# Performance work log

Hardware: AMD Instinct MI355X
Metric: run time of the kernel (lower is better)

The kernel has to match this reference:

```python
import jax, jax.numpy as jnp
import numpy as np

P_SCALE = 5.0
Q_SCALE = 0.3
EPS = 1e-06
NORM_EPS = 1e-12


def stack3x3_same(img):
    """im2col for 3x3 kernel, 'same' zero padding, stride 1.
    img: (B,H,W,C) -> (B,H,W,9,C), tap order row-major (dy,dx) in {-1,0,1}^2,
    matching the TF stack3x3 ordering with clip=0, pad=1."""
    B, H, W, C = img.shape
    padded = jnp.pad(img, ((0, 0), (1, 1), (1, 1), (0, 0)))
    taps = [padded[:, dy:dy + H, dx:dx + W, :] for dy in range(3) for dx in range(3)]
    return jnp.stack(taps, axis=3)


def setup_inputs() -> dict:
    key = jax.random.key(0)
    k1, k2 = jax.random.split(key)
    B, H, W, C = 32, 64, 64, 64
    n_kernels, ksize = 128, 3
    inputs = jax.random.normal(k1, (B, H, W, C), dtype=jnp.float32)
    # glorot-uniform-ish weight, shape (1, C*k*k, n_kernels)
    fan_in = C * ksize * ksize
    limit = np.sqrt(6.0 / (fan_in + n_kernels)).astype(np.float32)
    w = jax.random.uniform(k2, (1, fan_in, n_kernels), dtype=jnp.float32,
                           minval=-limit, maxval=limit)
    p = jnp.full((n_kernels,), 0.7 * P_SCALE, dtype=jnp.float32)
    q = jnp.full((1,), 1.0 * Q_SCALE, dtype=jnp.float32)
    return {"inputs": inputs, "w": w, "p": p, "q": q}


def reference(inputs, w, p, q):
    B, H, W, C = inputs.shape
    n_kernels = w.shape[-1]
    ksq = w.shape[1] // C  # kernel_size^2 = 9

    # im2col: (B, H*W, C*9), tap-major flatten (matches tf stack axis=3 + reshape)
    x = stack3x3_same(inputs).reshape(B, H * W, ksq * C)

    p_eff = jnp.exp(p / P_SCALE)            # (n_kernels,)
    q_eff = jnp.exp(-q / Q_SCALE)           # (1,)

    # L2 norms (sqrt of clamped square-sum), matching l2_normal
    x_norm = jnp.sqrt(jnp.maximum(jnp.sum(x * x, axis=2, keepdims=True), NORM_EPS)) + q_eff
    w_norm = jnp.sqrt(jnp.maximum(jnp.sum(w * w, axis=1, keepdims=True), NORM_EPS))

    # cosine-similarity matmul: (B, HW, K) x (1, K, N) -> (B, HW, N)
    sim = jnp.einsum('bsk,kn->bsn', x / x_norm, (w / w_norm)[0])

    # sharpened rescaling: sign(x) * (|x| + eps)^p
    out = jnp.sign(sim) * jnp.power(jnp.abs(sim) + EPS, p_eff)
    return out.reshape(B, H, W, n_kernels)
```

## Files before the change

kernel.cpp:

```cpp
#include <hip/hip_runtime.h>
#include <hip/hip_bf16.h>


typedef short bf16x8 __attribute__((ext_vector_type(8)));
typedef float f32x4 __attribute__((ext_vector_type(4)));

__device__ __forceinline__ unsigned short f2bf(float f) {
    union { float f; unsigned int u; } v; v.f = f;
    unsigned int u = v.u;
    unsigned int r = (u + 0x7fffu + ((u >> 16) & 1u)) >> 16;
    return (unsigned short)r;
}

__global__ void prep_w_kernel(const float* __restrict__ w,
                              unsigned short* __restrict__ wn2) {
    const int n = blockIdx.x;
    const int lane = threadIdx.x;
    float vals[9];
    float s = 0.f;
#pragma unroll
    for (int i = 0; i < 9; ++i) {
        float v = w[(i * 64 + lane) * 128 + n];
        vals[i] = v;
        s += v * v;
    }
#pragma unroll
    for (int off = 1; off < 64; off <<= 1) s += __shfl_xor(s, off);
    const float inv = 1.0f / sqrtf(fmaxf(s, 1e-12f));
    const int kc = lane >> 5, koff = lane & 31;
#pragma unroll
    for (int i = 0; i < 9; ++i)
        wn2[((i * 2 + kc) * 128 + n) * 32 + koff] = f2bf(vals[i] * inv);
}

__global__ __launch_bounds__(256, 4) void cossim_main(
    const float* __restrict__ in, const unsigned short* __restrict__ wn,
    const float* __restrict__ p, const float* __restrict__ q,
    float* __restrict__ out) {
    __shared__ unsigned short A[4 * 66 * 72];
    __shared__ float rcsum[256];
    __shared__ float xni[128];
    __shared__ float pfs[128];

    const int tid = (int)threadIdx.x;
    const int l = ((int)blockIdx.x & 7) * 128 + ((int)blockIdx.x >> 3);
    const int b = l >> 5, y0 = (l & 31) * 2;

    if (tid < 128) pfs[tid] = expf(p[tid] * 0.2f);

    {
        const int r = tid >> 6;
        const int col = tid & 63;
        const int row = y0 + r - 1;
        unsigned short* dst = &A[(r * 66 + col + 1) * 72];
        float s = 0.f;
        if ((unsigned)row < 64u) {
            const float4* src = reinterpret_cast<const float4*>(
                in + (size_t)b * 262144 + row * 4096 + col * 64);
#pragma unroll
            for (int it = 0; it < 8; ++it) {
                float4 v0 = src[2 * it];
                float4 v1 = src[2 * it + 1];
                s += v0.x * v0.x + v0.y * v0.y + v0.z * v0.z + v0.w * v0.w;
                s += v1.x * v1.x + v1.y * v1.y + v1.z * v1.z + v1.w * v1.w;
                union { float f; unsigned u; } ux, uy, uz, uw;
                uint4 pk;
                ux.f = v0.x; uy.f = v0.y; uz.f = v0.z; uw.f = v0.w;
                pk.x = __builtin_amdgcn_perm(uy.u + 0x8000u, ux.u + 0x8000u, 0x07060302u);
                pk.y = __builtin_amdgcn_perm(uw.u + 0x8000u, uz.u + 0x8000u, 0x07060302u);
                ux.f = v1.x; uy.f = v1.y; uz.f = v1.z; uw.f = v1.w;
                pk.z = __builtin_amdgcn_perm(uy.u + 0x8000u, ux.u + 0x8000u, 0x07060302u);
                pk.w = __builtin_amdgcn_perm(uw.u + 0x8000u, uz.u + 0x8000u, 0x07060302u);
                *reinterpret_cast<uint4*>(dst + it * 8) = pk;
            }
        } else {
            uint4 z; z.x = z.y = z.z = z.w = 0u;
#pragma unroll
            for (int it = 0; it < 8; ++it)
                *reinterpret_cast<uint4*>(dst + it * 8) = z;
        }
        rcsum[tid] = s;
    }
    if (tid < 64) {
        const int r = tid >> 4, side = (tid >> 3) & 1, ch = (tid & 7) * 8;
        uint4 z; z.x = z.y = z.z = z.w = 0u;
        *reinterpret_cast<uint4*>(&A[(r * 66 + side * 65) * 72 + ch]) = z;
    }
    __syncthreads();

    if (tid < 128) {
        const int ry = tid >> 6, x = tid & 63;
        const float qe = expf(q[0] * (-1.0f / 0.3f));
        float s = 0.f;
#pragma unroll
        for (int dy = 0; dy < 3; ++dy) {
            const float* rs = &rcsum[(ry + dy) * 64];
            if (x > 0) s += rs[x - 1];
            s += rs[x];
            if (x < 63) s += rs[x + 1];
        }
        xni[tid] = 1.0f / (sqrtf(fmaxf(s, 1e-12f)) + qe);
    }
    __syncthreads();

    const int wv = tid >> 6, lane = tid & 63;
    const int lr = lane & 15, lg = lane >> 4;
    const int wm = wv >> 1, wnh = wv & 1;
    f32x4 acc[4][4] = {};
    const unsigned short* wB = wn + (wnh * 64 + lr) * 32 + lg * 8;

    bf16x8 bc0 = *reinterpret_cast<const bf16x8*>(wB);
    bf16x8 bc1 = *reinterpret_cast<const bf16x8*>(wB + 512);
    bf16x8 bc2 = *reinterpret_cast<const bf16x8*>(wB + 1024);
    bf16x8 bc3 = *reinterpret_cast<const bf16x8*>(wB + 1536);

#pragma unroll
    for (int s = 0; s < 18; ++s) {
        bf16x8 bn0, bn1, bn2, bn3;
        if (s + 1 < 18) {
            const unsigned short* wt = wB + (s + 1) * 4096;
            bn0 = *reinterpret_cast<const bf16x8*>(wt);
            bn1 = *reinterpret_cast<const bf16x8*>(wt + 512);
            bn2 = *reinterpret_cast<const bf16x8*>(wt + 1024);
            bn3 = *reinterpret_cast<const bf16x8*>(wt + 1536);
        }
        const int dy = s / 6, dx = (s >> 1) % 3, kc = s & 1;
        const unsigned short* abase =
            &A[((wm + dy) * 66 + lr + dx) * 72 + kc * 32 + lg * 8];
#pragma unroll
        for (int mf = 0; mf < 4; ++mf) {
            bf16x8 av = *reinterpret_cast<const bf16x8*>(abase + mf * 16 * 72);
            acc[mf][0] = __builtin_amdgcn_mfma_f32_16x16x32_bf16(av, bc0, acc[mf][0], 0, 0, 0);
            acc[mf][1] = __builtin_amdgcn_mfma_f32_16x16x32_bf16(av, bc1, acc[mf][1], 0, 0, 0);
            acc[mf][2] = __builtin_amdgcn_mfma_f32_16x16x32_bf16(av, bc2, acc[mf][2], 0, 0, 0);
            acc[mf][3] = __builtin_amdgcn_mfma_f32_16x16x32_bf16(av, bc3, acc[mf][3], 0, 0, 0);
        }
        bc0 = bn0; bc1 = bn1; bc2 = bn2; bc3 = bn3;
    }

    float* orow = out + ((size_t)(b * 64 + y0 + wm) * 64) * 128;
#pragma unroll
    for (int mf = 0; mf < 4; ++mf) {
#pragma unroll
        for (int i = 0; i < 4; ++i) {
            const int pix = mf * 16 + lg * 4 + i;
            const float xn = xni[wm * 64 + pix];
#pragma unroll
            for (int nf = 0; nf < 4; ++nf) {
                const int n = wnh * 64 + nf * 16 + lr;
                float sim = acc[mf][nf][i] * xn;
                float aa = fabsf(sim) + 1e-6f;
                float r = exp2f(pfs[n] * log2f(aa));
                orow[(size_t)pix * 128 + n] = copysignf(r, sim);
            }
        }
    }
}

extern "C" void kernel_launch(void* const* d_in, const int* in_sizes, int n_in,
                              void* d_out, int out_size, void* d_ws, size_t ws_size,
                              hipStream_t stream) {
    (void)in_sizes; (void)n_in; (void)out_size; (void)ws_size;
    const float* in = (const float*)d_in[0];
    const float* w  = (const float*)d_in[1];
    const float* p  = (const float*)d_in[2];
    const float* q  = (const float*)d_in[3];
    float* out = (float*)d_out;
    unsigned short* wn = (unsigned short*)d_ws;

    prep_w_kernel<<<128, 64, 0, stream>>>(w, wn);
    cossim_main<<<1024, 256, 0, stream>>>(in, wn, p, q, out);
}
```

Measured before the change: 43.35 us.

## Use two waves per block with each wave computing both rows

Halves the block to 128 threads. Each wave now covers both output rows (8 M-fragments) for one 64-column half of the output channels, instead of one row per wave. Each weight fragment is reused across twice as many A fragments, which cuts global weight loads per MFMA. The cost is a doubled accumulator (128 floats per lane), so register pressure rises and occupancy falls, and the staging loop runs twice per thread.

```diff
diff --git a/kernel.cpp b/kernel.cpp
--- a/kernel.cpp
+++ b/kernel.cpp
@@ -33,7 +33,7 @@
         wn2[((i * 2 + kc) * 128 + n) * 32 + koff] = f2bf(vals[i] * inv);
 }
 
-__global__ __launch_bounds__(256, 4) void cossim_main(
+__global__ __launch_bounds__(128, 2) void cossim_main(
     const float* __restrict__ in, const unsigned short* __restrict__ wn,
     const float* __restrict__ p, const float* __restrict__ q,
     float* __restrict__ out) {
@@ -46,11 +46,13 @@
     const int l = ((int)blockIdx.x & 7) * 128 + ((int)blockIdx.x >> 3);
     const int b = l >> 5, y0 = (l & 31) * 2;
 
-    if (tid < 128) pfs[tid] = expf(p[tid] * 0.2f);
+    pfs[tid] = expf(p[tid] * 0.2f);
 
-    {
-        const int r = tid >> 6;
-        const int col = tid & 63;
+#pragma unroll
+    for (int u2 = 0; u2 < 2; ++u2) {
+        const int u = tid + u2 * 128;
+        const int r = u >> 6;
+        const int col = u & 63;
         const int row = y0 + r - 1;
         unsigned short* dst = &A[(r * 66 + col + 1) * 72];
         float s = 0.f;
@@ -79,7 +81,7 @@
             for (int it = 0; it < 8; ++it)
                 *reinterpret_cast<uint4*>(dst + it * 8) = z;
         }
-        rcsum[tid] = s;
+        rcsum[u] = s;
     }
     if (tid < 64) {
         const int r = tid >> 4, side = (tid >> 3) & 1, ch = (tid & 7) * 8;
@@ -88,7 +90,7 @@
     }
     __syncthreads();
 
-    if (tid < 128) {
+    {
         const int ry = tid >> 6, x = tid & 63;
         const float qe = expf(q[0] * (-1.0f / 0.3f));
         float s = 0.f;
@@ -105,9 +107,8 @@
 
     const int wv = tid >> 6, lane = tid & 63;
     const int lr = lane & 15, lg = lane >> 4;
-    const int wm = wv >> 1, wnh = wv & 1;
-    f32x4 acc[4][4] = {};
-    const unsigned short* wB = wn + (wnh * 64 + lr) * 32 + lg * 8;
+    f32x4 acc[8][4] = {};
+    const unsigned short* wB = wn + (wv * 64 + lr) * 32 + lg * 8;
 
     bf16x8 bc0 = *reinterpret_cast<const bf16x8*>(wB);
     bf16x8 bc1 = *reinterpret_cast<const bf16x8*>(wB + 512);
@@ -125,11 +126,12 @@
             bn3 = *reinterpret_cast<const bf16x8*>(wt + 1536);
         }
         const int dy = s / 6, dx = (s >> 1) % 3, kc = s & 1;
-        const unsigned short* abase =
-            &A[((wm + dy) * 66 + lr + dx) * 72 + kc * 32 + lg * 8];
 #pragma unroll
-        for (int mf = 0; mf < 4; ++mf) {
-            bf16x8 av = *reinterpret_cast<const bf16x8*>(abase + mf * 16 * 72);
+        for (int mf = 0; mf < 8; ++mf) {
+            const unsigned short* ap =
+                &A[(((mf >> 2) + dy) * 66 + (mf & 3) * 16 + lr + dx) * 72
+                   + kc * 32 + lg * 8];
+            bf16x8 av = *reinterpret_cast<const bf16x8*>(ap);
             acc[mf][0] = __builtin_amdgcn_mfma_f32_16x16x32_bf16(av, bc0, acc[mf][0], 0, 0, 0);
             acc[mf][1] = __builtin_amdgcn_mfma_f32_16x16x32_bf16(av, bc1, acc[mf][1], 0, 0, 0);
             acc[mf][2] = __builtin_amdgcn_mfma_f32_16x16x32_bf16(av, bc2, acc[mf][2], 0, 0, 0);
@@ -138,20 +140,22 @@
         bc0 = bn0; bc1 = bn1; bc2 = bn2; bc3 = bn3;
     }
 
-    float* orow = out + ((size_t)(b * 64 + y0 + wm) * 64) * 128;
+    const float* pf = &pfs[wv * 64];
 #pragma unroll
-    for (int mf = 0; mf < 4; ++mf) {
+    for (int mf = 0; mf < 8; ++mf) {
+        float* orow = out + ((size_t)(b * 64 + y0 + (mf >> 2)) * 64) * 128 + wv * 64;
 #pragma unroll
         for (int i = 0; i < 4; ++i) {
             const int pix = mf * 16 + lg * 4 + i;
-            const float xn = xni[wm * 64 + pix];
+            const int px = pix & 63;
+            const float xn = xni[pix];
 #pragma unroll
             for (int nf = 0; nf < 4; ++nf) {
-                const int n = wnh * 64 + nf * 16 + lr;
+                const int n = nf * 16 + lr;
                 float sim = acc[mf][nf][i] * xn;
                 float aa = fabsf(sim) + 1e-6f;
-                float r = exp2f(pfs[n] * log2f(aa));
-                orow[(size_t)pix * 128 + n] = copysignf(r, sim);
+                float r = exp2f(pf[n] * log2f(aa));
+                orow[(size_t)px * 128 + n] = copysignf(r, sim);
             }
         }
     }
@@ -169,5 +173,5 @@
     unsigned short* wn = (unsigned short*)d_ws;
 
     prep_w_kernel<<<128, 64, 0, stream>>>(w, wn);
-    cossim_main<<<1024, 256, 0, stream>>>(in, wn, p, q, out);
+    cossim_main<<<1024, 128, 0, stream>>>(in, wn, p, q, out);
 }
```

Result: slower. 51.21 us (+18.1%).

## Split output channels across blocks and stage output through LDS for coalesced stores

Applied to the files above, without the earlier changes.

Each block now handles only half of the 128 output channels, doubling the grid to 2048 blocks and halving the accumulator registers per wave. Results are staged in shared memory (reusing the A tile buffer) and then written with float4 stores covering contiguous 64-channel rows, in place of scattered scalar stores. The cost is that every input tile is loaded, converted to bf16 and norm-reduced twice, once per channel-half block, and two extra barriers are added.

```diff
diff --git a/kernel.cpp b/kernel.cpp
--- a/kernel.cpp
+++ b/kernel.cpp
@@ -33,20 +33,25 @@
         wn2[((i * 2 + kc) * 128 + n) * 32 + koff] = f2bf(vals[i] * inv);
 }
 
+#define OBLD 68
+
 __global__ __launch_bounds__(256, 4) void cossim_main(
     const float* __restrict__ in, const unsigned short* __restrict__ wn,
     const float* __restrict__ p, const float* __restrict__ q,
     float* __restrict__ out) {
-    __shared__ unsigned short A[4 * 66 * 72];
+    __shared__ __align__(16) unsigned char smemRaw[4 * 66 * 72 * 2];
+    unsigned short* A = reinterpret_cast<unsigned short*>(smemRaw);
+    float* OB = reinterpret_cast<float*>(smemRaw);
     __shared__ float rcsum[256];
     __shared__ float xni[128];
-    __shared__ float pfs[128];
+    __shared__ float pfs[64];
 
     const int tid = (int)threadIdx.x;
-    const int l = ((int)blockIdx.x & 7) * 128 + ((int)blockIdx.x >> 3);
-    const int b = l >> 5, y0 = (l & 31) * 2;
+    const int l = ((int)blockIdx.x & 7) * 256 + ((int)blockIdx.x >> 3);
+    const int sp = l >> 1, nh = l & 1;
+    const int b = sp >> 5, y0 = (sp & 31) * 2;
 
-    if (tid < 128) pfs[tid] = expf(p[tid] * 0.2f);
+    if (tid < 64) pfs[tid] = expf(p[nh * 64 + tid] * 0.2f);
 
     {
         const int r = tid >> 6;
@@ -105,55 +110,61 @@
 
     const int wv = tid >> 6, lane = tid & 63;
     const int lr = lane & 15, lg = lane >> 4;
-    const int wm = wv >> 1, wnh = wv & 1;
-    f32x4 acc[4][4] = {};
-    const unsigned short* wB = wn + (wnh * 64 + lr) * 32 + lg * 8;
+    const int wm = wv >> 1, wq = wv & 1;
+    f32x4 acc[4][2] = {};
+    const unsigned short* wB = wn + (nh * 64 + wq * 32 + lr) * 32 + lg * 8;
 
     bf16x8 bc0 = *reinterpret_cast<const bf16x8*>(wB);
     bf16x8 bc1 = *reinterpret_cast<const bf16x8*>(wB + 512);
-    bf16x8 bc2 = *reinterpret_cast<const bf16x8*>(wB + 1024);
-    bf16x8 bc3 = *reinterpret_cast<const bf16x8*>(wB + 1536);
 
 #pragma unroll
     for (int s = 0; s < 18; ++s) {
-        bf16x8 bn0, bn1, bn2, bn3;
+        bf16x8 bn0, bn1;
         if (s + 1 < 18) {
             const unsigned short* wt = wB + (s + 1) * 4096;
             bn0 = *reinterpret_cast<const bf16x8*>(wt);
             bn1 = *reinterpret_cast<const bf16x8*>(wt + 512);
-            bn2 = *reinterpret_cast<const bf16x8*>(wt + 1024);
-            bn3 = *reinterpret_cast<const bf16x8*>(wt + 1536);
         }
         const int dy = s / 6, dx = (s >> 1) % 3, kc = s & 1;
-        const unsigned short* abase =
-            &A[((wm + dy) * 66 + lr + dx) * 72 + kc * 32 + lg * 8];
 #pragma unroll
         for (int mf = 0; mf < 4; ++mf) {
-            bf16x8 av = *reinterpret_cast<const bf16x8*>(abase + mf * 16 * 72);
+            const unsigned short* ap =
+                &A[((wm + dy) * 66 + mf * 16 + lr + dx) * 72 + kc * 32 + lg * 8];
+            bf16x8 av = *reinterpret_cast<const bf16x8*>(ap);
             acc[mf][0] = __builtin_amdgcn_mfma_f32_16x16x32_bf16(av, bc0, acc[mf][0], 0, 0, 0);
             acc[mf][1] = __builtin_amdgcn_mfma_f32_16x16x32_bf16(av, bc1, acc[mf][1], 0, 0, 0);
-            acc[mf][2] = __builtin_amdgcn_mfma_f32_16x16x32_bf16(av, bc2, acc[mf][2], 0, 0, 0);
-            acc[mf][3] = __builtin_amdgcn_mfma_f32_16x16x32_bf16(av, bc3, acc[mf][3], 0, 0, 0);
         }
-        bc0 = bn0; bc1 = bn1; bc2 = bn2; bc3 = bn3;
+        bc0 = bn0; bc1 = bn1;
     }
+    __syncthreads();
 
-    float* orow = out + ((size_t)(b * 64 + y0 + wm) * 64) * 128;
+    const float* pf = pfs;
 #pragma unroll
     for (int mf = 0; mf < 4; ++mf) {
 #pragma unroll
         for (int i = 0; i < 4; ++i) {
-            const int pix = mf * 16 + lg * 4 + i;
-            const float xn = xni[wm * 64 + pix];
+            const int pix = wm * 64 + mf * 16 + lg * 4 + i;
+            const float xn = xni[pix];
 #pragma unroll
-            for (int nf = 0; nf < 4; ++nf) {
-                const int n = wnh * 64 + nf * 16 + lr;
+            for (int nf = 0; nf < 2; ++nf) {
+                const int nl = wq * 32 + nf * 16 + lr;
                 float sim = acc[mf][nf][i] * xn;
                 float aa = fabsf(sim) + 1e-6f;
-                float r = exp2f(pfs[n] * log2f(aa));
-                orow[(size_t)pix * 128 + n] = copysignf(r, sim);
+                float r = exp2f(pf[nl] * log2f(aa));
+                OB[pix * OBLD + nl] = copysignf(r, sim);
             }
         }
+    }
+    __syncthreads();
+
+#pragma unroll
+    for (int j = 0; j < 8; ++j) {
+        const int f = tid + 256 * j;
+        const int px = f >> 4, c = f & 15;
+        float4 v = *reinterpret_cast<const float4*>(&OB[px * OBLD + c * 4]);
+        const int row = y0 + (px >> 6), col = px & 63;
+        *reinterpret_cast<float4*>(
+            out + ((size_t)((b * 64 + row) * 64 + col)) * 128 + nh * 64 + c * 4) = v;
     }
 }
 
@@ -169,5 +180,5 @@
     unsigned short* wn = (unsigned short*)d_ws;
 
     prep_w_kernel<<<128, 64, 0, stream>>>(w, wn);
-    cossim_main<<<1024, 256, 0, stream>>>(in, wn, p, q, out);
+    cossim_main<<<2048, 256, 0, stream>>>(in, wn, p, q, out);
 }
```

Result: slower. 50.54 us (+16.6%).
